# Performance work log

Measured on AMD Instinct MI355X. Metric: run time of the kernel, lower is better.

The kernel has to match this reference:

```python
import jax, jax.numpy as jnp
import numpy as np

N = 50000
E = 800000
H = 2          # heads
C = 64         # out channels per head (embedding_size)
NEG_SLOPE = 0.2


def setup_inputs() -> dict:
    key = jax.random.key(0)
    ks = jax.random.split(key, 8)
    x = jax.random.normal(ks[0], (N, 1), dtype=jnp.float32)
    edge_index = jax.random.randint(ks[1], (2, E), 0, N, dtype=jnp.int64)
    edge_attr = jax.random.normal(ks[2], (E, 1), dtype=jnp.float32)
    # GATv2Conv params: lin_l, lin_r (with bias), lin_edge (no bias), att, out bias
    W_l = jax.random.normal(ks[3], (1, H * C), dtype=jnp.float32)
    b_l = jnp.zeros((H * C,), dtype=jnp.float32)
    W_r = jax.random.normal(ks[4], (1, H * C), dtype=jnp.float32)
    b_r = jnp.zeros((H * C,), dtype=jnp.float32)
    W_e = jax.random.normal(ks[5], (1, H * C), dtype=jnp.float32)
    att = jax.random.normal(ks[6], (H, C), dtype=jnp.float32)
    bias = jnp.zeros((H * C,), dtype=jnp.float32)
    return {"x": x, "edge_index": edge_index, "edge_attr": edge_attr,
            "W_l": W_l, "b_l": b_l, "W_r": W_r, "b_r": b_r,
            "W_e": W_e, "att": att, "bias": bias}


def reference(x, edge_index, edge_attr, W_l, b_l, W_r, b_r, W_e, att, bias):
    n = x.shape[0]
    src, dst = edge_index[0], edge_index[1]

    # add_self_loops=True with fill_value='mean': self-loop edge_attr at node i
    # is the mean of incoming edge_attr (0 if no incoming edges).
    attr_sum = jax.ops.segment_sum(edge_attr, dst, num_segments=n)      # [N,1]
    cnt = jax.ops.segment_sum(jnp.ones((src.shape[0], 1), edge_attr.dtype), dst, num_segments=n)
    loop_attr = attr_sum / jnp.maximum(cnt, 1.0)                         # [N,1]

    loop = jnp.arange(n, dtype=src.dtype)
    src_f = jnp.concatenate([src, loop])                                 # [E+N]
    dst_f = jnp.concatenate([dst, loop])
    attr_f = jnp.concatenate([edge_attr, loop_attr], axis=0)             # [E+N,1]

    x_l = (x @ W_l + b_l).reshape(n, H, C)    # source transform
    x_r = (x @ W_r + b_r).reshape(n, H, C)    # target transform
    e = (attr_f @ W_e).reshape(-1, H, C)      # edge feature embedding

    # GATv2 attention: leaky_relu(x_l[j] + x_r[i] + e) . att
    g = jax.nn.leaky_relu(x_l[src_f] + x_r[dst_f] + e, NEG_SLOPE)        # [E+N,H,C]
    logits = jnp.einsum('ehc,hc->eh', g, att)                            # [E+N,H]

    # segment softmax grouped by destination node
    mx = jax.ops.segment_max(logits, dst_f, num_segments=n)              # [N,H]
    a = jnp.exp(logits - mx[dst_f])
    den = jax.ops.segment_sum(a, dst_f, num_segments=n)                  # [N,H]
    alpha = a / den[dst_f]                                               # [E+N,H]

    # weighted scatter-add of source messages
    out = jax.ops.segment_sum(alpha[:, :, None] * x_l[src_f], dst_f, num_segments=n)  # [N,H,C]
    return out.reshape(n, H * C) + bias
```

## Files before the change

### kernel.cpp

```cpp
#include <hip/hip_runtime.h>

#define NEG 0.2f

typedef float f4v __attribute__((ext_vector_type(4)));

__device__ __forceinline__ float leaky(float v){ return fmaxf(v, NEG * v); }

__global__ void __launch_bounds__(256, 6) k_edge(
        const int* __restrict__ src, const int* __restrict__ dst,
        const float* __restrict__ attr, const float* __restrict__ x,
        const float* __restrict__ Wl, const float* __restrict__ Wr,
        const float* __restrict__ We, const float* __restrict__ bl,
        const float* __restrict__ br, const float* __restrict__ att,
        int* __restrict__ head, int* __restrict__ nxt,
        float4* __restrict__ payload, int E){
    const int ln = threadIdx.x & 15;
    const float4* Wl4 = (const float4*)Wl;
    const float4* Wr4 = (const float4*)Wr;
    const float4* We4 = (const float4*)We;
    const float4* bl4 = (const float4*)bl;
    const float4* br4 = (const float4*)br;
    const float4* at4 = (const float4*)att;
    const int q = ln * 2;
    float4 wl0 = Wl4[q], wl1 = Wl4[q+1];
    float4 wr0 = Wr4[q], wr1 = Wr4[q+1];
    float4 we0 = We4[q], we1 = We4[q+1];
    float4 b0  = bl4[q], b1  = bl4[q+1];
    float4 c0  = br4[q], c1  = br4[q+1];
    float4 a0  = at4[q], a1  = at4[q+1];
    b0.x += c0.x; b0.y += c0.y; b0.z += c0.z; b0.w += c0.w;
    b1.x += c1.x; b1.y += c1.y; b1.z += c1.z; b1.w += c1.w;

    const int gid  = (blockIdx.x * 256 + threadIdx.x) >> 4;
    const int base = gid * 16;
    if (base >= E) return;

    const int eL = base + ln;
    const bool val = eL < E;
    int   sL = 0, dL = 0;
    float aL = 0.f;
    if (val){ sL = src[eL]; dL = dst[eL]; aL = attr[eL]; }
    float xsL = val ? x[sL] : 0.f;
    float xdL = val ? x[dL] : 0.f;
    int prevL = 0;
    if (val)
        prevL = atomicExch(&head[dL * 16 + ln], eL);

    const int cnt = min(16, E - base);
    float l0L = 0.f, l1L = 0.f;
    for (int j = 0; j < cnt; ++j){
        float xs = __shfl(xsL, j, 16);
        float xd = __shfl(xdL, j, 16);
        float a  = __shfl(aL,  j, 16);
        float acc;
        {
            float v0 = fmaf(xs, wl0.x, fmaf(xd, wr0.x, fmaf(a, we0.x, b0.x)));
            float v1 = fmaf(xs, wl0.y, fmaf(xd, wr0.y, fmaf(a, we0.y, b0.y)));
            float v2 = fmaf(xs, wl0.z, fmaf(xd, wr0.z, fmaf(a, we0.z, b0.z)));
            float v3 = fmaf(xs, wl0.w, fmaf(xd, wr0.w, fmaf(a, we0.w, b0.w)));
            acc  = leaky(v0) * a0.x;
            acc  = fmaf(leaky(v1), a0.y, acc);
            acc  = fmaf(leaky(v2), a0.z, acc);
            acc  = fmaf(leaky(v3), a0.w, acc);
            v0 = fmaf(xs, wl1.x, fmaf(xd, wr1.x, fmaf(a, we1.x, b1.x)));
            v1 = fmaf(xs, wl1.y, fmaf(xd, wr1.y, fmaf(a, we1.y, b1.y)));
            v2 = fmaf(xs, wl1.z, fmaf(xd, wr1.z, fmaf(a, we1.z, b1.z)));
            v3 = fmaf(xs, wl1.w, fmaf(xd, wr1.w, fmaf(a, we1.w, b1.w)));
            acc  = fmaf(leaky(v0), a1.x, acc);
            acc  = fmaf(leaky(v1), a1.y, acc);
            acc  = fmaf(leaky(v2), a1.z, acc);
            acc  = fmaf(leaky(v3), a1.w, acc);
        }
        acc += __shfl_xor(acc, 1);
        acc += __shfl_xor(acc, 2);
        acc += __shfl_xor(acc, 4);
        float other = __shfl_xor(acc, 8);
        if (ln == j){
            l0L = (j < 8) ? acc : other;
            l1L = (j < 8) ? other : acc;
        }
    }
    if (val){
        f4v pv = { xsL, aL, l0L, l1L };
        __builtin_nontemporal_store(pv, (f4v*)&payload[eL]);
        __builtin_nontemporal_store(prevL, &nxt[eL]);
    }
}

__global__ void __launch_bounds__(256, 6) k_walk(
        const float* __restrict__ x,
        const int* __restrict__ head, const int* __restrict__ nxt,
        const float4* __restrict__ payload,
        const float* __restrict__ Wl, const float* __restrict__ Wr,
        const float* __restrict__ We, const float* __restrict__ bl,
        const float* __restrict__ br, const float* __restrict__ att,
        const float* __restrict__ bias,
        float4* __restrict__ out, int N){
    int t = blockIdx.x * 256 + threadIdx.x;
    int i = t >> 4, ln = t & 15;
    if (i >= N) return;

    const float4* Wl4 = (const float4*)Wl;
    const float4* Wr4 = (const float4*)Wr;
    const float4* We4 = (const float4*)We;
    const float4* bl4 = (const float4*)bl;
    const float4* br4 = (const float4*)br;
    const float4* at4 = (const float4*)att;
    const int q = ln * 2;
    float4 wl0 = Wl4[q], wl1 = Wl4[q+1];
    float4 wr0 = Wr4[q], wr1 = Wr4[q+1];
    float4 we0 = We4[q], we1 = We4[q+1];
    float4 b0  = bl4[q], b1  = bl4[q+1];
    float4 c0  = br4[q], c1  = br4[q+1];
    float4 a0  = at4[q], a1  = at4[q+1];
    wl0.x += wr0.x; wl0.y += wr0.y; wl0.z += wr0.z; wl0.w += wr0.w;
    wl1.x += wr1.x; wl1.y += wr1.y; wl1.z += wr1.z; wl1.w += wr1.w;
    b0.x += c0.x; b0.y += c0.y; b0.z += c0.z; b0.w += c0.w;
    b1.x += c1.x; b1.y += c1.y; b1.z += c1.z; b1.w += c1.w;

    float m0 = -3.4e38f, d0 = 0.f, n0 = 0.f;
    float m1 = -3.4e38f, d1 = 0.f, n1 = 0.f;
    float asum = 0.f;
    int deg = 0;
    for (int e = head[(size_t)i * 16 + ln]; e >= 0; e = nxt[e]){
        float4 v = payload[e];
        ++deg;
        asum += v.y;
        float mn0 = fmaxf(m0, v.z);
        float s0 = __expf(m0 - mn0), p0 = __expf(v.z - mn0);
        d0 = fmaf(d0, s0, p0);
        n0 = fmaf(n0, s0, p0 * v.x);
        m0 = mn0;
        float mn1 = fmaxf(m1, v.w);
        float s1 = __expf(m1 - mn1), p1 = __expf(v.w - mn1);
        d1 = fmaf(d1, s1, p1);
        n1 = fmaf(n1, s1, p1 * v.x);
        m1 = mn1;
    }
    #pragma unroll
    for (int off = 1; off < 16; off <<= 1){
        float om0 = __shfl_xor(m0, off), od0 = __shfl_xor(d0, off), on0 = __shfl_xor(n0, off);
        float om1 = __shfl_xor(m1, off), od1 = __shfl_xor(d1, off), on1 = __shfl_xor(n1, off);
        asum += __shfl_xor(asum, off);
        deg  += __shfl_xor(deg, off);
        float mn = fmaxf(m0, om0);
        d0 = d0 * __expf(m0 - mn) + od0 * __expf(om0 - mn);
        n0 = n0 * __expf(m0 - mn) + on0 * __expf(om0 - mn);
        m0 = mn;
        mn = fmaxf(m1, om1);
        d1 = d1 * __expf(m1 - mn) + od1 * __expf(om1 - mn);
        n1 = n1 * __expf(m1 - mn) + on1 * __expf(om1 - mn);
        m1 = mn;
    }
    float xi = x[i];
    float la = asum / (float)max(deg, 1);
    float pl;
    {
        float v0 = fmaf(xi, wl0.x, fmaf(la, we0.x, b0.x));
        float v1 = fmaf(xi, wl0.y, fmaf(la, we0.y, b0.y));
        float v2 = fmaf(xi, wl0.z, fmaf(la, we0.z, b0.z));
        float v3 = fmaf(xi, wl0.w, fmaf(la, we0.w, b0.w));
        pl  = leaky(v0) * a0.x;
        pl  = fmaf(leaky(v1), a0.y, pl);
        pl  = fmaf(leaky(v2), a0.z, pl);
        pl  = fmaf(leaky(v3), a0.w, pl);
        v0 = fmaf(xi, wl1.x, fmaf(la, we1.x, b1.x));
        v1 = fmaf(xi, wl1.y, fmaf(la, we1.y, b1.y));
        v2 = fmaf(xi, wl1.z, fmaf(la, we1.z, b1.z));
        v3 = fmaf(xi, wl1.w, fmaf(la, we1.w, b1.w));
        pl  = fmaf(leaky(v0), a1.x, pl);
        pl  = fmaf(leaky(v1), a1.y, pl);
        pl  = fmaf(leaky(v2), a1.z, pl);
        pl  = fmaf(leaky(v3), a1.w, pl);
    }
    pl += __shfl_xor(pl, 1);
    pl += __shfl_xor(pl, 2);
    pl += __shfl_xor(pl, 4);
    float other = __shfl_xor(pl, 8);
    float l0 = (ln < 8) ? pl : other;
    float l1 = (ln < 8) ? other : pl;
    {
        float mn = fmaxf(m0, l0);
        float s = __expf(m0 - mn), p = __expf(l0 - mn);
        d0 = fmaf(d0, s, p);
        n0 = fmaf(n0, s, p * xi);
    }
    {
        float mn = fmaxf(m1, l1);
        float s = __expf(m1 - mn), p = __expf(l1 - mn);
        d1 = fmaf(d1, s, p);
        n1 = fmaf(n1, s, p * xi);
    }
    float sres0 = n0 / d0;
    float sres1 = n1 / d1;

    float4 w0 = Wl4[ln],      w1 = Wl4[ln + 16];
    float4 g0 = bl4[ln],      g1 = bl4[ln + 16];
    float4 z0 = ((const float4*)bias)[ln], z1 = ((const float4*)bias)[ln + 16];
    float4* orow = out + (size_t)i * 32;
    orow[ln]      = make_float4(fmaf(sres0, w0.x, g0.x + z0.x),
                                fmaf(sres0, w0.y, g0.y + z0.y),
                                fmaf(sres0, w0.z, g0.z + z0.z),
                                fmaf(sres0, w0.w, g0.w + z0.w));
    orow[ln + 16] = make_float4(fmaf(sres1, w1.x, g1.x + z1.x),
                                fmaf(sres1, w1.y, g1.y + z1.y),
                                fmaf(sres1, w1.z, g1.z + z1.z),
                                fmaf(sres1, w1.w, g1.w + z1.w));
}

extern "C" void kernel_launch(void* const* d_in, const int* in_sizes, int n_in,
                              void* d_out, int out_size, void* d_ws, size_t ws_size,
                              hipStream_t stream) {
    const float* x    = (const float*)d_in[0];
    const int*   ei   = (const int*)  d_in[1];
    const float* attr = (const float*)d_in[2];
    const float* Wl   = (const float*)d_in[3];
    const float* bl   = (const float*)d_in[4];
    const float* Wr   = (const float*)d_in[5];
    const float* br   = (const float*)d_in[6];
    const float* We   = (const float*)d_in[7];
    const float* att  = (const float*)d_in[8];
    const float* bias = (const float*)d_in[9];
    float* out = (float*)d_out;

    const int N = in_sizes[0];
    const int E = in_sizes[2];
    const int* src = ei;
    const int* dst = ei + E;

    char* w = (char*)d_ws;
    float4* payload = (float4*)w;
    int*    nxt     = (int*)(w + (size_t)E * 16);
    int*    head    = nxt + E;

    hipMemsetAsync(head, 0xFF, (size_t)16 * N * sizeof(int), stream);

    int egroups = (E + 15) / 16;
    int eblocks = (egroups + 15) / 16;
    k_edge<<<eblocks, 256, 0, stream>>>(src, dst, attr, x,
                                        Wl, Wr, We, bl, br, att,
                                        head, nxt, payload, E);
    k_walk<<<((size_t)16 * N + 255) / 256, 256, 0, stream>>>(x, head, nxt, payload,
                                                             Wl, Wr, We, bl, br, att, bias,
                                                             (float4*)out, N);
}
```

Measured before the change: 79.43 us.

## Replace per-node linked lists with bucketed edge scatter and block-local shared-memory softmax

```diff
diff --git a/kernel.cpp b/kernel.cpp
--- a/kernel.cpp
+++ b/kernel.cpp
@@ -1,20 +1,77 @@
 #include <hip/hip_runtime.h>
 
 #define NEG 0.2f
-
-typedef float f4v __attribute__((ext_vector_type(4)));
+#define CAP 6144
+#define EPB 2048
 
 __device__ __forceinline__ float leaky(float v){ return fmaxf(v, NEG * v); }
 
-__global__ void __launch_bounds__(256, 6) k_edge(
+__device__ __forceinline__ unsigned fmap(float f){
+    unsigned b = __float_as_uint(f);
+    return (b & 0x80000000u) ? ~b : (b | 0x80000000u);
+}
+__device__ __forceinline__ float funmap(unsigned u){
+    return (u & 0x80000000u) ? __uint_as_float(u & 0x7fffffffu) : __uint_as_float(~u);
+}
+
+__global__ void __launch_bounds__(256) k_init(int* __restrict__ gcur, int nb){
+    int t = blockIdx.x * 256 + threadIdx.x;
+    if (t < nb) gcur[t] = t * CAP;
+}
+
+__global__ void __launch_bounds__(256) k_scatter(
         const int* __restrict__ src, const int* __restrict__ dst,
         const float* __restrict__ attr, const float* __restrict__ x,
+        int* __restrict__ gcur, float4* __restrict__ sorted, int E, int nb){
+    __shared__ int hist[256];
+    __shared__ int cur[256];
+    const int tid = threadIdx.x;
+    for (int k = tid; k < nb; k += 256) hist[k] = 0;
+    __syncthreads();
+    const int base = blockIdx.x * EPB;
+    const int lim  = min(EPB, E - base);
+    for (int k = tid; k < lim; k += 256)
+        atomicAdd(&hist[dst[base + k] >> 8], 1);
+    __syncthreads();
+    for (int k = tid; k < nb; k += 256){
+        int c = hist[k];
+        cur[k] = c ? atomicAdd(&gcur[k], c) : 0;
+    }
+    __syncthreads();
+    for (int k = tid; k < lim; k += 256){
+        int e = base + k;
+        int d = dst[e];
+        int b = d >> 8;
+        int pos = atomicAdd(&cur[b], 1);
+        if (pos < (b + 1) * CAP)
+            sorted[pos] = make_float4(x[src[e]], x[d], attr[e],
+                                      __int_as_float(d & 255));
+    }
+}
+
+__global__ void __launch_bounds__(1024) k_node(
+        const float* __restrict__ x,
+        const int* __restrict__ gcur, const float4* __restrict__ sorted,
         const float* __restrict__ Wl, const float* __restrict__ Wr,
         const float* __restrict__ We, const float* __restrict__ bl,
         const float* __restrict__ br, const float* __restrict__ att,
-        int* __restrict__ head, int* __restrict__ nxt,
-        float4* __restrict__ payload, int E){
-    const int ln = threadIdx.x & 15;
+        const float* __restrict__ bias,
+        float4* __restrict__ out, int N){
+    __shared__ unsigned mm[256][2];
+    __shared__ float    dd[256][2];
+    __shared__ float    nn[256][2];
+    __shared__ float    as_[256];
+    __shared__ int      dg[256];
+    const int tid = threadIdx.x;
+    const int b   = blockIdx.x;
+    if (tid < 256){
+        mm[tid][0] = 0u;  mm[tid][1] = 0u;
+        dd[tid][0] = 0.f; dd[tid][1] = 0.f;
+        nn[tid][0] = 0.f; nn[tid][1] = 0.f;
+        as_[tid] = 0.f;   dg[tid] = 0;
+    }
+
+    const int ln = tid & 15;
     const float4* Wl4 = (const float4*)Wl;
     const float4* Wr4 = (const float4*)Wr;
     const float4* We4 = (const float4*)We;
@@ -30,182 +87,145 @@
     float4 a0  = at4[q], a1  = at4[q+1];
     b0.x += c0.x; b0.y += c0.y; b0.z += c0.z; b0.w += c0.w;
     b1.x += c1.x; b1.y += c1.y; b1.z += c1.z; b1.w += c1.w;
-
-    const int gid  = (blockIdx.x * 256 + threadIdx.x) >> 4;
-    const int base = gid * 16;
-    if (base >= E) return;
-
-    const int eL = base + ln;
-    const bool val = eL < E;
-    int   sL = 0, dL = 0;
-    float aL = 0.f;
-    if (val){ sL = src[eL]; dL = dst[eL]; aL = attr[eL]; }
-    float xsL = val ? x[sL] : 0.f;
-    float xdL = val ? x[dL] : 0.f;
-    int prevL = 0;
-    if (val)
-        prevL = atomicExch(&head[dL * 16 + ln], eL);
-
-    const int cnt = min(16, E - base);
-    float l0L = 0.f, l1L = 0.f;
-    for (int j = 0; j < cnt; ++j){
-        float xs = __shfl(xsL, j, 16);
-        float xd = __shfl(xdL, j, 16);
-        float a  = __shfl(aL,  j, 16);
-        float acc;
+    __syncthreads();
+
+    int cnt = gcur[b] - b * CAP;
+    if (cnt > CAP) cnt = CAP;
+    const float4* bucket = sorted + (size_t)b * CAP;
+
+    float l0s[6], l1s[6], xss[6], aas[6];
+    int   nds[6];
+    #pragma unroll
+    for (int p = 0; p < 6; ++p){
+        int idx = p * 1024 + tid;
+        bool val = idx < cnt;
+        float4 f4 = val ? bucket[idx] : make_float4(0.f, 0.f, 0.f, 0.f);
+        float xsL = f4.x, xdL = f4.y, aL = f4.z;
+        int node = val ? (__float_as_int(f4.w) & 255) : -1;
+        float l0L = 0.f, l1L = 0.f;
+        for (int j = 0; j < 16; ++j){
+            float xs = __shfl(xsL, j, 16);
+            float xd = __shfl(xdL, j, 16);
+            float a  = __shfl(aL,  j, 16);
+            float acc;
+            {
+                float v0 = fmaf(xs, wl0.x, fmaf(xd, wr0.x, fmaf(a, we0.x, b0.x)));
+                float v1 = fmaf(xs, wl0.y, fmaf(xd, wr0.y, fmaf(a, we0.y, b0.y)));
+                float v2 = fmaf(xs, wl0.z, fmaf(xd, wr0.z, fmaf(a, we0.z, b0.z)));
+                float v3 = fmaf(xs, wl0.w, fmaf(xd, wr0.w, fmaf(a, we0.w, b0.w)));
+                acc  = leaky(v0) * a0.x;
+                acc  = fmaf(leaky(v1), a0.y, acc);
+                acc  = fmaf(leaky(v2), a0.z, acc);
+                acc  = fmaf(leaky(v3), a0.w, acc);
+                v0 = fmaf(xs, wl1.x, fmaf(xd, wr1.x, fmaf(a, we1.x, b1.x)));
+                v1 = fmaf(xs, wl1.y, fmaf(xd, wr1.y, fmaf(a, we1.y, b1.y)));
+                v2 = fmaf(xs, wl1.z, fmaf(xd, wr1.z, fmaf(a, we1.z, b1.z)));
+                v3 = fmaf(xs, wl1.w, fmaf(xd, wr1.w, fmaf(a, we1.w, b1.w)));
+                acc  = fmaf(leaky(v0), a1.x, acc);
+                acc  = fmaf(leaky(v1), a1.y, acc);
+                acc  = fmaf(leaky(v2), a1.z, acc);
+                acc  = fmaf(leaky(v3), a1.w, acc);
+            }
+            acc += __shfl_xor(acc, 1);
+            acc += __shfl_xor(acc, 2);
+            acc += __shfl_xor(acc, 4);
+            float other = __shfl_xor(acc, 8);
+            if (ln == j){
+                l0L = (j < 8) ? acc : other;
+                l1L = (j < 8) ? other : acc;
+            }
+        }
+        if (val){
+            atomicMax(&mm[node][0], fmap(l0L));
+            atomicMax(&mm[node][1], fmap(l1L));
+        }
+        l0s[p] = l0L; l1s[p] = l1L; xss[p] = xsL; aas[p] = aL; nds[p] = node;
+    }
+    __syncthreads();
+
+    #pragma unroll
+    for (int p = 0; p < 6; ++p){
+        int node = nds[p];
+        if (node >= 0){
+            float m0 = funmap(mm[node][0]);
+            float m1 = funmap(mm[node][1]);
+            float p0 = __expf(l0s[p] - m0);
+            float p1 = __expf(l1s[p] - m1);
+            atomicAdd(&dd[node][0], p0);
+            atomicAdd(&nn[node][0], p0 * xss[p]);
+            atomicAdd(&dd[node][1], p1);
+            atomicAdd(&nn[node][1], p1 * xss[p]);
+            atomicAdd(&as_[node], aas[p]);
+            atomicAdd(&dg[node], 1);
+        }
+    }
+    __syncthreads();
+
+    const int grp = tid >> 4;
+    float4 ww0 = Wl4[ln],  ww1 = Wl4[ln + 16];
+    float4 gg0 = bl4[ln],  gg1 = bl4[ln + 16];
+    float4 z0  = ((const float4*)bias)[ln], z1 = ((const float4*)bias)[ln + 16];
+    #pragma unroll
+    for (int qq = 0; qq < 4; ++qq){
+        int node = qq * 64 + grp;
+        int i = b * 256 + node;
+        if (i >= N) continue;
+        int   degv = dg[node];
+        float m0 = degv ? funmap(mm[node][0]) : -3.4e38f;
+        float m1 = degv ? funmap(mm[node][1]) : -3.4e38f;
+        float d0 = dd[node][0], n0 = nn[node][0];
+        float d1 = dd[node][1], n1 = nn[node][1];
+        float la = as_[node] / (float)max(degv, 1);
+        float xi = x[i];
+        float pl;
         {
-            float v0 = fmaf(xs, wl0.x, fmaf(xd, wr0.x, fmaf(a, we0.x, b0.x)));
-            float v1 = fmaf(xs, wl0.y, fmaf(xd, wr0.y, fmaf(a, we0.y, b0.y)));
-            float v2 = fmaf(xs, wl0.z, fmaf(xd, wr0.z, fmaf(a, we0.z, b0.z)));
-            float v3 = fmaf(xs, wl0.w, fmaf(xd, wr0.w, fmaf(a, we0.w, b0.w)));
-            acc  = leaky(v0) * a0.x;
-            acc  = fmaf(leaky(v1), a0.y, acc);
-            acc  = fmaf(leaky(v2), a0.z, acc);
-            acc  = fmaf(leaky(v3), a0.w, acc);
-            v0 = fmaf(xs, wl1.x, fmaf(xd, wr1.x, fmaf(a, we1.x, b1.x)));
-            v1 = fmaf(xs, wl1.y, fmaf(xd, wr1.y, fmaf(a, we1.y, b1.y)));
-            v2 = fmaf(xs, wl1.z, fmaf(xd, wr1.z, fmaf(a, we1.z, b1.z)));
-            v3 = fmaf(xs, wl1.w, fmaf(xd, wr1.w, fmaf(a, we1.w, b1.w)));
-            acc  = fmaf(leaky(v0), a1.x, acc);
-            acc  = fmaf(leaky(v1), a1.y, acc);
-            acc  = fmaf(leaky(v2), a1.z, acc);
-            acc  = fmaf(leaky(v3), a1.w, acc);
-        }
-        acc += __shfl_xor(acc, 1);
-        acc += __shfl_xor(acc, 2);
-        acc += __shfl_xor(acc, 4);
-        float other = __shfl_xor(acc, 8);
-        if (ln == j){
-            l0L = (j < 8) ? acc : other;
-            l1L = (j < 8) ? other : acc;
-        }
-    }
-    if (val){
-        f4v pv = { xsL, aL, l0L, l1L };
-        __builtin_nontemporal_store(pv, (f4v*)&payload[eL]);
-        __builtin_nontemporal_store(prevL, &nxt[eL]);
-    }
-}
-
-__global__ void __launch_bounds__(256, 6) k_walk(
-        const float* __restrict__ x,
-        const int* __restrict__ head, const int* __restrict__ nxt,
-        const float4* __restrict__ payload,
-        const float* __restrict__ Wl, const float* __restrict__ Wr,
-        const float* __restrict__ We, const float* __restrict__ bl,
-        const float* __restrict__ br, const float* __restrict__ att,
-        const float* __restrict__ bias,
-        float4* __restrict__ out, int N){
-    int t = blockIdx.x * 256 + threadIdx.x;
-    int i = t >> 4, ln = t & 15;
-    if (i >= N) return;
-
-    const float4* Wl4 = (const float4*)Wl;
-    const float4* Wr4 = (const float4*)Wr;
-    const float4* We4 = (const float4*)We;
-    const float4* bl4 = (const float4*)bl;
-    const float4* br4 = (const float4*)br;
-    const float4* at4 = (const float4*)att;
-    const int q = ln * 2;
-    float4 wl0 = Wl4[q], wl1 = Wl4[q+1];
-    float4 wr0 = Wr4[q], wr1 = Wr4[q+1];
-    float4 we0 = We4[q], we1 = We4[q+1];
-    float4 b0  = bl4[q], b1  = bl4[q+1];
-    float4 c0  = br4[q], c1  = br4[q+1];
-    float4 a0  = at4[q], a1  = at4[q+1];
-    wl0.x += wr0.x; wl0.y += wr0.y; wl0.z += wr0.z; wl0.w += wr0.w;
-    wl1.x += wr1.x; wl1.y += wr1.y; wl1.z += wr1.z; wl1.w += wr1.w;
-    b0.x += c0.x; b0.y += c0.y; b0.z += c0.z; b0.w += c0.w;
-    b1.x += c1.x; b1.y += c1.y; b1.z += c1.z; b1.w += c1.w;
-
-    float m0 = -3.4e38f, d0 = 0.f, n0 = 0.f;
-    float m1 = -3.4e38f, d1 = 0.f, n1 = 0.f;
-    float asum = 0.f;
-    int deg = 0;
-    for (int e = head[(size_t)i * 16 + ln]; e >= 0; e = nxt[e]){
-        float4 v = payload[e];
-        ++deg;
-        asum += v.y;
-        float mn0 = fmaxf(m0, v.z);
-        float s0 = __expf(m0 - mn0), p0 = __expf(v.z - mn0);
-        d0 = fmaf(d0, s0, p0);
-        n0 = fmaf(n0, s0, p0 * v.x);
-        m0 = mn0;
-        float mn1 = fmaxf(m1, v.w);
-        float s1 = __expf(m1 - mn1), p1 = __expf(v.w - mn1);
-        d1 = fmaf(d1, s1, p1);
-        n1 = fmaf(n1, s1, p1 * v.x);
-        m1 = mn1;
-    }
-    #pragma unroll
-    for (int off = 1; off < 16; off <<= 1){
-        float om0 = __shfl_xor(m0, off), od0 = __shfl_xor(d0, off), on0 = __shfl_xor(n0, off);
-        float om1 = __shfl_xor(m1, off), od1 = __shfl_xor(d1, off), on1 = __shfl_xor(n1, off);
-        asum += __shfl_xor(asum, off);
-        deg  += __shfl_xor(deg, off);
-        float mn = fmaxf(m0, om0);
-        d0 = d0 * __expf(m0 - mn) + od0 * __expf(om0 - mn);
-        n0 = n0 * __expf(m0 - mn) + on0 * __expf(om0 - mn);
-        m0 = mn;
-        mn = fmaxf(m1, om1);
-        d1 = d1 * __expf(m1 - mn) + od1 * __expf(om1 - mn);
-        n1 = n1 * __expf(m1 - mn) + on1 * __expf(om1 - mn);
-        m1 = mn;
-    }
-    float xi = x[i];
-    float la = asum / (float)max(deg, 1);
-    float pl;
-    {
-        float v0 = fmaf(xi, wl0.x, fmaf(la, we0.x, b0.x));
-        float v1 = fmaf(xi, wl0.y, fmaf(la, we0.y, b0.y));
-        float v2 = fmaf(xi, wl0.z, fmaf(la, we0.z, b0.z));
-        float v3 = fmaf(xi, wl0.w, fmaf(la, we0.w, b0.w));
-        pl  = leaky(v0) * a0.x;
-        pl  = fmaf(leaky(v1), a0.y, pl);
-        pl  = fmaf(leaky(v2), a0.z, pl);
-        pl  = fmaf(leaky(v3), a0.w, pl);
-        v0 = fmaf(xi, wl1.x, fmaf(la, we1.x, b1.x));
-        v1 = fmaf(xi, wl1.y, fmaf(la, we1.y, b1.y));
-        v2 = fmaf(xi, wl1.z, fmaf(la, we1.z, b1.z));
-        v3 = fmaf(xi, wl1.w, fmaf(la, we1.w, b1.w));
-        pl  = fmaf(leaky(v0), a1.x, pl);
-        pl  = fmaf(leaky(v1), a1.y, pl);
-        pl  = fmaf(leaky(v2), a1.z, pl);
-        pl  = fmaf(leaky(v3), a1.w, pl);
-    }
-    pl += __shfl_xor(pl, 1);
-    pl += __shfl_xor(pl, 2);
-    pl += __shfl_xor(pl, 4);
-    float other = __shfl_xor(pl, 8);
-    float l0 = (ln < 8) ? pl : other;
-    float l1 = (ln < 8) ? other : pl;
-    {
-        float mn = fmaxf(m0, l0);
-        float s = __expf(m0 - mn), p = __expf(l0 - mn);
-        d0 = fmaf(d0, s, p);
-        n0 = fmaf(n0, s, p * xi);
-    }
-    {
-        float mn = fmaxf(m1, l1);
-        float s = __expf(m1 - mn), p = __expf(l1 - mn);
-        d1 = fmaf(d1, s, p);
-        n1 = fmaf(n1, s, p * xi);
-    }
-    float sres0 = n0 / d0;
-    float sres1 = n1 / d1;
-
-    float4 w0 = Wl4[ln],      w1 = Wl4[ln + 16];
-    float4 g0 = bl4[ln],      g1 = bl4[ln + 16];
-    float4 z0 = ((const float4*)bias)[ln], z1 = ((const float4*)bias)[ln + 16];
-    float4* orow = out + (size_t)i * 32;
-    orow[ln]      = make_float4(fmaf(sres0, w0.x, g0.x + z0.x),
-                                fmaf(sres0, w0.y, g0.y + z0.y),
-                                fmaf(sres0, w0.z, g0.z + z0.z),
-                                fmaf(sres0, w0.w, g0.w + z0.w));
-    orow[ln + 16] = make_float4(fmaf(sres1, w1.x, g1.x + z1.x),
-                                fmaf(sres1, w1.y, g1.y + z1.y),
-                                fmaf(sres1, w1.z, g1.z + z1.z),
-                                fmaf(sres1, w1.w, g1.w + z1.w));
+            float v0 = fmaf(xi, wl0.x + wr0.x, fmaf(la, we0.x, b0.x));
+            float v1 = fmaf(xi, wl0.y + wr0.y, fmaf(la, we0.y, b0.y));
+            float v2 = fmaf(xi, wl0.z + wr0.z, fmaf(la, we0.z, b0.z));
+            float v3 = fmaf(xi, wl0.w + wr0.w, fmaf(la, we0.w, b0.w));
+            pl  = leaky(v0) * a0.x;
+            pl  = fmaf(leaky(v1), a0.y, pl);
+            pl  = fmaf(leaky(v2), a0.z, pl);
+            pl  = fmaf(leaky(v3), a0.w, pl);
+            v0 = fmaf(xi, wl1.x + wr1.x, fmaf(la, we1.x, b1.x));
+            v1 = fmaf(xi, wl1.y + wr1.y, fmaf(la, we1.y, b1.y));
+            v2 = fmaf(xi, wl1.z + wr1.z, fmaf(la, we1.z, b1.z));
+            v3 = fmaf(xi, wl1.w + wr1.w, fmaf(la, we1.w, b1.w));
+            pl  = fmaf(leaky(v0), a1.x, pl);
+            pl  = fmaf(leaky(v1), a1.y, pl);
+            pl  = fmaf(leaky(v2), a1.z, pl);
+            pl  = fmaf(leaky(v3), a1.w, pl);
+        }
+        pl += __shfl_xor(pl, 1);
+        pl += __shfl_xor(pl, 2);
+        pl += __shfl_xor(pl, 4);
+        float other = __shfl_xor(pl, 8);
+        float l0 = (ln < 8) ? pl : other;
+        float l1 = (ln < 8) ? other : pl;
+        {
+            float mn = fmaxf(m0, l0);
+            float s = __expf(m0 - mn), p = __expf(l0 - mn);
+            d0 = fmaf(d0, s, p);
+            n0 = fmaf(n0, s, p * xi);
+        }
+        {
+            float mn = fmaxf(m1, l1);
+            float s = __expf(m1 - mn), p = __expf(l1 - mn);
+            d1 = fmaf(d1, s, p);
+            n1 = fmaf(n1, s, p * xi);
+        }
+        float sres0 = n0 / d0;
+        float sres1 = n1 / d1;
+        float4* orow = out + (size_t)i * 32;
+        orow[ln]      = make_float4(fmaf(sres0, ww0.x, gg0.x + z0.x),
+                                    fmaf(sres0, ww0.y, gg0.y + z0.y),
+                                    fmaf(sres0, ww0.z, gg0.z + z0.z),
+                                    fmaf(sres0, ww0.w, gg0.w + z0.w));
+        orow[ln + 16] = make_float4(fmaf(sres1, ww1.x, gg1.x + z1.x),
+                                    fmaf(sres1, ww1.y, gg1.y + z1.y),
+                                    fmaf(sres1, ww1.z, gg1.z + z1.z),
+                                    fmaf(sres1, ww1.w, gg1.w + z1.w));
+    }
 }
 
 extern "C" void kernel_launch(void* const* d_in, const int* in_sizes, int n_in,
@@ -228,19 +248,16 @@
     const int* src = ei;
     const int* dst = ei + E;
 
+    const int nb = (N + 255) >> 8;
+
     char* w = (char*)d_ws;
-    float4* payload = (float4*)w;
-    int*    nxt     = (int*)(w + (size_t)E * 16);
-    int*    head    = nxt + E;
-
-    hipMemsetAsync(head, 0xFF, (size_t)16 * N * sizeof(int), stream);
-
-    int egroups = (E + 15) / 16;
-    int eblocks = (egroups + 15) / 16;
-    k_edge<<<eblocks, 256, 0, stream>>>(src, dst, attr, x,
-                                        Wl, Wr, We, bl, br, att,
-                                        head, nxt, payload, E);
-    k_walk<<<((size_t)16 * N + 255) / 256, 256, 0, stream>>>(x, head, nxt, payload,
-                                                             Wl, Wr, We, bl, br, att, bias,
-                                                             (float4*)out, N);
-}
+    float4* sorted = (float4*)w;
+    int*    gcur   = (int*)(w + (size_t)nb * CAP * 16);
+
+    k_init<<<(nb + 255) / 256, 256, 0, stream>>>(gcur, nb);
+    k_scatter<<<(E + EPB - 1) / EPB, 256, 0, stream>>>(src, dst, attr, x,
+                                                       gcur, sorted, E, nb);
+    k_node<<<nb, 1024, 0, stream>>>(x, gcur, sorted,
+                                    Wl, Wr, We, bl, br, att, bias,
+                                    (float4*)out, N);
+}
```

Result: slower. 104.9 us (+32.1%).
